# Kernel tuning notes

Measured on AMD Instinct MI355X. Metric: run time of the kernel, lower is better.

Reference implementation:

```python
import jax, jax.numpy as jnp
import numpy as np

B, S, E, H = 2, 2048, 1024, 16
DH = E // H
SCALE = 1.0 / float(np.sqrt(E))  # note: original scales by 1/sqrt(hidden_dim), not head_dim


def _icl_mask(s):
    # triu(diagonal=0) is masked (-inf): only strictly-past positions visible,
    # except (0,0) which is explicitly unmasked so row 0 attends to itself.
    m = jnp.triu(jnp.ones((s, s), dtype=bool), k=0)
    return m.at[0, 0].set(False)


def setup_inputs() -> dict:
    key = jax.random.key(0)
    ks = jax.random.split(key, 7)
    mk = lambda k, shp: jax.random.normal(k, shp, dtype=jnp.float32)
    return {
        "q": mk(ks[0], (B, S, E)),
        "k": mk(ks[1], (B, S, E)),
        "v": mk(ks[2], (B, S, E)),
        "Wq": mk(ks[3], (E, E)) * 0.02,
        "Wk": mk(ks[4], (E, E)) * 0.02,
        "Wv": mk(ks[5], (E, E)) * 0.02,
        "Wo": mk(ks[6], (E, E)) * 0.02,
    }


def reference(q, k, v, Wq, Wk, Wv, Wo):
    b, s, e = q.shape
    h, dh = H, e // H
    # projections (nn.Linear: x @ W.T), split heads -> [b, h, s, dh]
    qh = (q @ Wq.T).reshape(b, s, h, dh).transpose(0, 2, 1, 3)
    kh = (k @ Wk.T).reshape(b, s, h, dh).transpose(0, 2, 1, 3)
    vh = (v @ Wv.T).reshape(b, s, h, dh).transpose(0, 2, 1, 3)
    scores = jnp.einsum("bhsd,bhtd->bhst", qh, kh) * SCALE  # [b,h,s,s]
    scores = jnp.where(_icl_mask(s), -jnp.inf, scores)
    probs = jax.nn.softmax(scores, axis=-1)
    out = jnp.einsum("bhst,bhtd->bhsd", probs, vh)
    out = out.transpose(0, 2, 1, 3).reshape(b, s, e)
    return out @ Wo.T
```

## Files before the change

### kernel.cpp

```cpp
#include <hip/hip_runtime.h>
#include <hip/hip_bf16.h>

typedef unsigned short u16;
typedef unsigned int u32;
typedef __bf16 bf16x8 __attribute__((ext_vector_type(8)));
typedef float float4_ __attribute__((ext_vector_type(4)));

#define B_ 2
#define S_ 2048
#define E_ 1024
#define H_ 16
#define DH_ 64
#define M_ (B_*S_)
#define E2_ (E_*E_)
#define SCALE_ 0.03125f
#define LOG2E_ 1.4426950408889634f

__device__ __forceinline__ u16 f2bf(float f) {
    unsigned int x = __float_as_uint(f);
    x += 0x7fffu + ((x >> 16) & 1u);
    return (u16)(x >> 16);
}

template <typename T> struct raw8;
template <> struct raw8<float> { float4_ lo, hi; };
template <> struct raw8<u16>   { bf16x8 v; };

__device__ __forceinline__ raw8<float> ldr8(const float* p) {
    raw8<float> r; const float4_* q = (const float4_*)p; r.lo = q[0]; r.hi = q[1]; return r;
}
__device__ __forceinline__ raw8<u16> ldr8(const u16* p) {
    raw8<u16> r; r.v = *(const bf16x8*)p; return r;
}
__device__ __forceinline__ bf16x8 cvt8(const raw8<u16>& r) { return r.v; }
__device__ __forceinline__ bf16x8 cvt8(const raw8<float>& r) {
    union { bf16x8 v; __hip_bfloat162 h[4]; } u;
    u.h[0] = __float22bfloat162_rn(float2{r.lo[0], r.lo[1]});
    u.h[1] = __float22bfloat162_rn(float2{r.lo[2], r.lo[3]});
    u.h[2] = __float22bfloat162_rn(float2{r.hi[0], r.hi[1]});
    u.h[3] = __float22bfloat162_rn(float2{r.hi[2], r.hi[3]});
    return u.v;
}
__device__ __forceinline__ bf16x8 ld8(const u16* p) { return *(const bf16x8*)p; }

__device__ __forceinline__ void async16(u16* lds, const u16* g) {
    __builtin_amdgcn_global_load_lds(
        (const __attribute__((address_space(1))) u32*)g,
        (__attribute__((address_space(3))) u32*)lds, 16, 0, 0);
}

__device__ __forceinline__ int swz32(int row, int col) {
    return row * 32 + ((((col >> 3) ^ (row & 3)) << 3) | (col & 7));
}

__global__ __launch_bounds__(256)
void conv_all_kernel(const float* __restrict__ q, const float* __restrict__ k,
                     const float* __restrict__ v,
                     const float* __restrict__ Wq, const float* __restrict__ Wk,
                     const float* __restrict__ Wv, const float* __restrict__ Wo,
                     u16* __restrict__ Xq, u16* __restrict__ Xk, u16* __restrict__ Xv,
                     u16* __restrict__ Wqb, u16* __restrict__ Wkb,
                     u16* __restrict__ Wvb, u16* __restrict__ Wob) {
    const int bid = blockIdx.x;
    const float* src;
    u16* dst;
    size_t base;
    if (bid < 6144) {
        const int which = bid >> 11, off = bid & 2047;
        src = which == 0 ? q : which == 1 ? k : v;
        dst = which == 0 ? Xq : which == 1 ? Xk : Xv;
        base = (size_t)off * 2048;
    } else {
        const int wb = bid - 6144;
        const int which = wb >> 9, off = wb & 511;
        src = which == 0 ? Wq : which == 1 ? Wk : which == 2 ? Wv : Wo;
        dst = which == 0 ? Wqb : which == 1 ? Wkb : which == 2 ? Wvb : Wob;
        base = (size_t)off * 2048;
    }
    const size_t i = base + (size_t)threadIdx.x * 8;
    *(bf16x8*)&dst[i] = cvt8(ldr8(&src[i]));
}

__global__ __launch_bounds__(256)
void proj_kernel(const u16* __restrict__ Xq, const u16* __restrict__ Xk, const u16* __restrict__ Xv,
                 const u16* __restrict__ Wqb, const u16* __restrict__ Wkb, const u16* __restrict__ Wvb,
                 u16* __restrict__ Qh, u16* __restrict__ Kh, u16* __restrict__ Vt) {
    const int z = blockIdx.z;
    const u16* A   = (z == 0) ? Xq : (z == 1) ? Xk : Xv;
    const u16* Wb  = (z == 0) ? Wqb : (z == 1) ? Wkb : Wvb;
    u16* C         = (z == 0) ? Qh : (z == 1) ? Kh : Vt;
    const float cscale = (z == 0) ? SCALE_ : 1.0f;
    const int transV = (z == 2);
    const int bm = blockIdx.x * 128, bn = blockIdx.y * 128;

    __shared__ u16 As[2][128 * 32];
    __shared__ u16 Bs[2][128 * 32];

    const int tid  = threadIdx.x;
    const int lane = tid & 63;
    const int w    = tid >> 6;
    const int wr   = (w >> 1) * 64, wc = (w & 1) * 64;
    const int m16  = lane & 15, quad = lane >> 4, q4 = quad * 4;

    const int row0 = tid >> 2, ch = tid & 3, row1 = row0 + 64;
    const int csw  = ((ch ^ (row0 & 3)) * 8);
    const u16* ag0 = &A[(size_t)(bm + row0) * 1024 + csw];
    const u16* ag1 = &A[(size_t)(bm + row1) * 1024 + csw];
    const u16* wg0 = &Wb[(size_t)(bn + row0) * 1024 + csw];
    const u16* wg1 = &Wb[(size_t)(bn + row1) * 1024 + csw];

    float4_ acc[4][4];
#pragma unroll
    for (int i = 0; i < 4; i++)
#pragma unroll
        for (int j = 0; j < 4; j++) acc[i][j] = (float4_){0.f, 0.f, 0.f, 0.f};

    async16((u16*)((char*)As[0] + (size_t)tid * 16), ag0);
    async16((u16*)((char*)As[0] + (size_t)tid * 16 + 4096), ag1);
    async16((u16*)((char*)Bs[0] + (size_t)tid * 16), wg0);
    async16((u16*)((char*)Bs[0] + (size_t)tid * 16 + 4096), wg1);
    __syncthreads();

    auto step = [&](int t, const u16* Asc, const u16* Bsc, u16* Asn, u16* Bsn) {
        if (t < 31) {
            const size_t ko = (size_t)(t + 1) * 32;
            async16((u16*)((char*)Asn + (size_t)tid * 16), ag0 + ko);
            async16((u16*)((char*)Asn + (size_t)tid * 16 + 4096), ag1 + ko);
            async16((u16*)((char*)Bsn + (size_t)tid * 16), wg0 + ko);
            async16((u16*)((char*)Bsn + (size_t)tid * 16 + 4096), wg1 + ko);
        }
        __builtin_amdgcn_sched_barrier(0);
        bf16x8 af[4], bfr[4];
#pragma unroll
        for (int rt = 0; rt < 4; rt++)
            af[rt] = *(const bf16x8*)&Asc[swz32(wr + rt * 16 + m16, quad * 8)];
#pragma unroll
        for (int ct = 0; ct < 4; ct++)
            bfr[ct] = *(const bf16x8*)&Bsc[swz32(wc + ct * 16 + m16, quad * 8)];
#pragma unroll
        for (int rt = 0; rt < 4; rt++)
#pragma unroll
            for (int ct = 0; ct < 4; ct++)
                acc[rt][ct] = __builtin_amdgcn_mfma_f32_16x16x32_bf16(af[rt], bfr[ct], acc[rt][ct], 0, 0, 0);
        if (t < 31) __syncthreads();
    };

    for (int t = 0; t < 32; t += 2) {
        step(t,     As[0], Bs[0], As[1], Bs[1]);
        step(t + 1, As[1], Bs[1], As[0], Bs[0]);
    }

#pragma unroll
    for (int rt = 0; rt < 4; rt++)
#pragma unroll
        for (int ct = 0; ct < 4; ct++)
#pragma unroll
            for (int r = 0; r < 4; r++) {
                int row = bm + wr + rt * 16 + q4 + r;
                int col = bn + wc + ct * 16 + m16;
                u16 val = f2bf(acc[rt][ct][r] * cscale);
                if (!transV) {
                    C[(size_t)row * 1024 + col] = val;
                } else {
                    int bb = row >> 11, s = row & 2047;
                    C[((size_t)(bb * 1024 + col)) * 2048 + s] = val;
                }
            }
}

__global__ __launch_bounds__(256)
void out_kernel(const u16* __restrict__ AO, const u16* __restrict__ Wob, float* __restrict__ C) {
    const int bm = blockIdx.x * 128, bn = blockIdx.y * 64;

    __shared__ u16 As[2][128 * 32];
    __shared__ u16 Bs[2][64 * 32];

    const int tid  = threadIdx.x;
    const int lane = tid & 63;
    const int w    = tid >> 6;
    const int m16  = lane & 15, quad = lane >> 4, q4 = quad * 4;
    const int c1   = tid + 256;

    const int swc = (((tid & 3) ^ ((tid >> 2) & 3)) * 8);
    const u16* ag0 = &AO[(size_t)(bm + (tid >> 2)) * 1024 + swc];
    const u16* ag1 = &AO[(size_t)(bm + (c1 >> 2)) * 1024 + swc];
    const u16* bg  = &Wob[(size_t)(bn + (tid >> 2)) * 1024 + swc];

    float4_ acc[2][4];
#pragma unroll
    for (int i = 0; i < 2; i++)
#pragma unroll
        for (int j = 0; j < 4; j++) acc[i][j] = (float4_){0.f, 0.f, 0.f, 0.f};

    async16((u16*)((char*)As[0] + (size_t)tid * 16), ag0);
    async16((u16*)((char*)As[0] + (size_t)c1 * 16), ag1);
    async16((u16*)((char*)Bs[0] + (size_t)tid * 16), bg);
    __syncthreads();

    auto step = [&](int t, const u16* Asc, const u16* Bsc, u16* Asn, u16* Bsn) {
        if (t < 31) {
            async16((u16*)((char*)Asn + (size_t)tid * 16), ag0 + (t + 1) * 32);
            async16((u16*)((char*)Asn + (size_t)c1 * 16), ag1 + (t + 1) * 32);
            async16((u16*)((char*)Bsn + (size_t)tid * 16), bg + (t + 1) * 32);
        }
        __builtin_amdgcn_sched_barrier(0);
        bf16x8 af[2], bfr[4];
#pragma unroll
        for (int rt = 0; rt < 2; rt++)
            af[rt] = *(const bf16x8*)&Asc[swz32(w * 32 + rt * 16 + m16, quad * 8)];
#pragma unroll
        for (int ct = 0; ct < 4; ct++)
            bfr[ct] = *(const bf16x8*)&Bsc[swz32(ct * 16 + m16, quad * 8)];
#pragma unroll
        for (int rt = 0; rt < 2; rt++)
#pragma unroll
            for (int ct = 0; ct < 4; ct++)
                acc[rt][ct] = __builtin_amdgcn_mfma_f32_16x16x32_bf16(af[rt], bfr[ct], acc[rt][ct], 0, 0, 0);
        if (t < 31) __syncthreads();
    };

    for (int t = 0; t < 32; t += 2) {
        step(t,     As[0], Bs[0], As[1], Bs[1]);
        step(t + 1, As[1], Bs[1], As[0], Bs[0]);
    }

#pragma unroll
    for (int rt = 0; rt < 2; rt++)
#pragma unroll
        for (int ct = 0; ct < 4; ct++)
#pragma unroll
            for (int r = 0; r < 4; r++) {
                int row = bm + w * 32 + rt * 16 + q4 + r;
                int col = bn + ct * 16 + m16;
                C[(size_t)row * 1024 + col] = acc[rt][ct][r];
            }
}

__device__ __forceinline__ int sw64(int row, int col) {
    return row * 64 + ((((col >> 3) ^ (row & 7)) << 3) | (col & 7));
}

__global__ __launch_bounds__(256, 2)
void attn_kernel(const u16* __restrict__ Qh, const u16* __restrict__ Kh,
                 const u16* __restrict__ Vt, u16* __restrict__ O) {
    const int h    = blockIdx.x;
    const int tq   = 31 - blockIdx.y;
    const int b    = blockIdx.z;
    const int tid  = threadIdx.x;
    const int lane = tid & 63;
    const int w    = tid >> 6;
    const int m16  = lane & 15;
    const int quad = lane >> 4;
    const int q4   = quad * 4;

    __shared__ u16 Ks[3][64 * 64];
    __shared__ u16 Vs[3][64 * 64];
    __shared__ u16 Ps[64 * 64];

    const int srow0 = tid >> 3;
    const int ssw   = (((tid & 7) ^ (srow0 & 7)) * 8);

    const size_t kbase = ((size_t)(b * S_)) * E_ + h * DH_;
    const size_t vbase = ((size_t)(b * 1024 + h * DH_)) * 2048;
    const u16* kg0 = &Kh[kbase + (size_t)srow0 * E_ + ssw];
    const u16* kg1 = kg0 + (size_t)32 * E_;
    const u16* vg0 = &Vt[vbase + (size_t)srow0 * 2048 + ssw];
    const u16* vg1 = vg0 + (size_t)32 * 2048;

    bf16x8 qf[2];
    {
        const u16* qa = Qh + ((size_t)(b * S_ + tq * 64 + w * 16 + m16)) * E_ + h * DH_;
        qf[0] = ld8(qa + quad * 8);
        qf[1] = ld8(qa + 32 + quad * 8);
    }

    float l_part[4] = {0.f, 0.f, 0.f, 0.f};
    float4_ o_acc[4];
#pragma unroll
    for (int dt = 0; dt < 4; dt++) o_acc[dt] = (float4_){0.f, 0.f, 0.f, 0.f};

    u16* k0 = &Ks[0][0]; u16* k1 = &Ks[1][0]; u16* k2 = &Ks[2][0];
    u16* v0 = &Vs[0][0]; u16* v1 = &Vs[1][0]; u16* v2 = &Vs[2][0];

    auto stage_to = [&](u16* kb, u16* vb, int tile) {
        const size_t ko = (size_t)tile * 64 * E_;
        const int    vo = tile * 64;
        async16(kb + tid * 8, kg0 + ko);
        async16(kb + (tid + 256) * 8, kg1 + ko);
        async16(vb + tid * 8, vg0 + vo);
        async16(vb + (tid + 256) * 8, vg1 + vo);
    };

    stage_to(k0, v0, 0);
    stage_to(k1, v1, tq > 0 ? 1 : 0);
    asm volatile("s_waitcnt vmcnt(4)" ::: "memory");
    __builtin_amdgcn_s_barrier();
    __builtin_amdgcn_sched_barrier(0);

    for (int t = 0; t <= tq; t++) {
        stage_to(k2, v2, (t + 2 <= tq) ? (t + 2) : tq);
        __builtin_amdgcn_sched_barrier(0);

        float4_ sc[4];
#pragma unroll
        for (int ct = 0; ct < 4; ct++) sc[ct] = (float4_){0.f, 0.f, 0.f, 0.f};
#pragma unroll
        for (int ks = 0; ks < 2; ks++)
#pragma unroll
            for (int ct = 0; ct < 4; ct++) {
                bf16x8 kf = *(const bf16x8*)&k0[sw64(ct * 16 + m16, ks * 32 + quad * 8)];
                sc[ct] = __builtin_amdgcn_mfma_f32_16x16x32_bf16(qf[ks], kf, sc[ct], 0, 0, 0);
            }

#pragma unroll
        for (int ct = 0; ct < 4; ct++) {
            float pp[4];
            if (t != tq) {
#pragma unroll
                for (int r = 0; r < 4; r++) {
                    pp[r] = exp2f(sc[ct][r] * LOG2E_);
                    l_part[r] += pp[r];
                }
            } else {
#pragma unroll
                for (int r = 0; r < 4; r++) {
                    int i_loc = w * 16 + q4 + r;
                    int j_loc = ct * 16 + m16;
                    bool allow = (j_loc < i_loc) || (tq == 0 && i_loc == 0 && j_loc == 0);
                    pp[r] = allow ? exp2f(sc[ct][r] * LOG2E_) : 0.f;
                    l_part[r] += pp[r];
                }
            }
            union { __hip_bfloat162 h2; u16 s[2]; } u01, u23;
            u01.h2 = __float22bfloat162_rn(float2{pp[0], pp[1]});
            u23.h2 = __float22bfloat162_rn(float2{pp[2], pp[3]});
            Ps[sw64(w * 16 + q4 + 0, ct * 16 + m16)] = u01.s[0];
            Ps[sw64(w * 16 + q4 + 1, ct * 16 + m16)] = u01.s[1];
            Ps[sw64(w * 16 + q4 + 2, ct * 16 + m16)] = u23.s[0];
            Ps[sw64(w * 16 + q4 + 3, ct * 16 + m16)] = u23.s[1];
        }

#pragma unroll
        for (int ks = 0; ks < 2; ks++) {
            bf16x8 pf = *(const bf16x8*)&Ps[sw64(w * 16 + m16, ks * 32 + quad * 8)];
#pragma unroll
            for (int dt = 0; dt < 4; dt++) {
                bf16x8 vf = *(const bf16x8*)&v0[sw64(dt * 16 + m16, ks * 32 + quad * 8)];
                o_acc[dt] = __builtin_amdgcn_mfma_f32_16x16x32_bf16(pf, vf, o_acc[dt], 0, 0, 0);
            }
        }

        asm volatile("s_waitcnt vmcnt(4)" ::: "memory");
        __builtin_amdgcn_s_barrier();
        __builtin_amdgcn_sched_barrier(0);

        u16* tk = k0; k0 = k1; k1 = k2; k2 = tk;
        u16* tv = v0; v0 = v1; v1 = v2; v2 = tv;
    }
    asm volatile("s_waitcnt vmcnt(0)" ::: "memory");

    const size_t obase = ((size_t)(b * S_ + tq * 64)) * E_ + h * DH_;
#pragma unroll
    for (int r = 0; r < 4; r++) {
        float l = l_part[r];
#pragma unroll
        for (int msk = 1; msk <= 8; msk <<= 1) l += __shfl_xor(l, msk);
        float inv_l = 1.0f / l;
        int row = w * 16 + q4 + r;
#pragma unroll
        for (int dt = 0; dt < 4; dt++) {
            int col = dt * 16 + m16;
            O[obase + (size_t)row * E_ + col] = f2bf(o_acc[dt][r] * inv_l);
        }
    }
}

extern "C" void kernel_launch(void* const* d_in, const int* in_sizes, int n_in,
                              void* d_out, int out_size, void* d_ws, size_t ws_size,
                              hipStream_t stream) {
    const float* q  = (const float*)d_in[0];
    const float* k  = (const float*)d_in[1];
    const float* v  = (const float*)d_in[2];
    const float* Wq = (const float*)d_in[3];
    const float* Wk = (const float*)d_in[4];
    const float* Wv = (const float*)d_in[5];
    const float* Wo = (const float*)d_in[6];

    const size_t ME = (size_t)M_ * E_;
    u16* ws  = (u16*)d_ws;
    u16* Qh  = ws;
    u16* Kh  = ws + ME;
    u16* Vt  = ws + 2 * ME;
    u16* AO  = ws + 3 * ME;
    u16* Wqb = AO;
    u16* Wkb = AO + E2_;
    u16* Wvb = AO + 2 * (size_t)E2_;
    u16* Wob = ws + 4 * ME;
    u16* Xv  = ws + 4 * ME + E2_;
    u16* Xq  = (u16*)d_out;
    u16* Xk  = Xq + ME;

    dim3 blk(256);
    conv_all_kernel<<<dim3(8192), blk, 0, stream>>>(q, k, v, Wq, Wk, Wv, Wo,
                                                    Xq, Xk, Xv, Wqb, Wkb, Wvb, Wob);
    proj_kernel<<<dim3(32, 8, 3), blk, 0, stream>>>(Xq, Xk, Xv, Wqb, Wkb, Wvb, Qh, Kh, Vt);
    attn_kernel<<<dim3(16, 32, 2), blk, 0, stream>>>(Qh, Kh, Vt, AO);
    out_kernel<<<dim3(32, 16), blk, 0, stream>>>(AO, Wob, (float*)d_out);
}
```

Baseline: 213.5 us.

## Process KV tiles in pairs with double-buffered pair staging in attention

The attention loop now handles two 64-wide KV tiles per iteration. K and V are staged as double-buffered pairs, and each tile gets its own P buffer, so there is one vmcnt wait and one barrier per pair instead of one per tile. The next pair's loads are issued at the start of each iteration and overlap with two tiles of QK/softmax/PV work. LDS use grows from about 56KB to 80KB per block, which could limit occupancy, and the wait is now a full vmcnt(0) rather than a partial one.

```diff
diff --git a/kernel.cpp b/kernel.cpp
--- a/kernel.cpp
+++ b/kernel.cpp
@@ -253,9 +253,9 @@
     const int quad = lane >> 4;
     const int q4   = quad * 4;
 
-    __shared__ u16 Ks[3][64 * 64];
-    __shared__ u16 Vs[3][64 * 64];
-    __shared__ u16 Ps[64 * 64];
+    __shared__ u16 Ks[2][2][64 * 64];
+    __shared__ u16 Vs[2][2][64 * 64];
+    __shared__ u16 Ps[2][64 * 64];
 
     const int srow0 = tid >> 3;
     const int ssw   = (((tid & 7) ^ (srow0 & 7)) * 8);
@@ -278,9 +278,6 @@
     float4_ o_acc[4];
 #pragma unroll
     for (int dt = 0; dt < 4; dt++) o_acc[dt] = (float4_){0.f, 0.f, 0.f, 0.f};
-
-    u16* k0 = &Ks[0][0]; u16* k1 = &Ks[1][0]; u16* k2 = &Ks[2][0];
-    u16* v0 = &Vs[0][0]; u16* v1 = &Vs[1][0]; u16* v2 = &Vs[2][0];
 
     auto stage_to = [&](u16* kb, u16* vb, int tile) {
         const size_t ko = (size_t)tile * 64 * E_;
@@ -290,28 +287,25 @@
         async16(vb + tid * 8, vg0 + vo);
         async16(vb + (tid + 256) * 8, vg1 + vo);
     };
-
-    stage_to(k0, v0, 0);
-    stage_to(k1, v1, tq > 0 ? 1 : 0);
-    asm volatile("s_waitcnt vmcnt(4)" ::: "memory");
-    __builtin_amdgcn_s_barrier();
-    __builtin_amdgcn_sched_barrier(0);
-
-    for (int t = 0; t <= tq; t++) {
-        stage_to(k2, v2, (t + 2 <= tq) ? (t + 2) : tq);
-        __builtin_amdgcn_sched_barrier(0);
-
-        float4_ sc[4];
+    auto stage_pair = [&](int pp, int t0) {
+        const int ta = (t0     < tq) ? t0     : tq;
+        const int tb = (t0 + 1 < tq) ? t0 + 1 : tq;
+        stage_to(&Ks[pp][0][0], &Vs[pp][0][0], ta);
+        stage_to(&Ks[pp][1][0], &Vs[pp][1][0], tb);
+    };
+
+    auto qk = [&](const u16* Kc, float4_* sc) {
 #pragma unroll
         for (int ct = 0; ct < 4; ct++) sc[ct] = (float4_){0.f, 0.f, 0.f, 0.f};
 #pragma unroll
         for (int ks = 0; ks < 2; ks++)
 #pragma unroll
             for (int ct = 0; ct < 4; ct++) {
-                bf16x8 kf = *(const bf16x8*)&k0[sw64(ct * 16 + m16, ks * 32 + quad * 8)];
+                bf16x8 kf = *(const bf16x8*)&Kc[sw64(ct * 16 + m16, ks * 32 + quad * 8)];
                 sc[ct] = __builtin_amdgcn_mfma_f32_16x16x32_bf16(qf[ks], kf, sc[ct], 0, 0, 0);
             }
-
+    };
+    auto sm = [&](const float4_* sc, u16* Pm, int t) {
 #pragma unroll
         for (int ct = 0; ct < 4; ct++) {
             float pp[4];
@@ -334,30 +328,53 @@
             union { __hip_bfloat162 h2; u16 s[2]; } u01, u23;
             u01.h2 = __float22bfloat162_rn(float2{pp[0], pp[1]});
             u23.h2 = __float22bfloat162_rn(float2{pp[2], pp[3]});
-            Ps[sw64(w * 16 + q4 + 0, ct * 16 + m16)] = u01.s[0];
-            Ps[sw64(w * 16 + q4 + 1, ct * 16 + m16)] = u01.s[1];
-            Ps[sw64(w * 16 + q4 + 2, ct * 16 + m16)] = u23.s[0];
-            Ps[sw64(w * 16 + q4 + 3, ct * 16 + m16)] = u23.s[1];
-        }
-
+            Pm[sw64(w * 16 + q4 + 0, ct * 16 + m16)] = u01.s[0];
+            Pm[sw64(w * 16 + q4 + 1, ct * 16 + m16)] = u01.s[1];
+            Pm[sw64(w * 16 + q4 + 2, ct * 16 + m16)] = u23.s[0];
+            Pm[sw64(w * 16 + q4 + 3, ct * 16 + m16)] = u23.s[1];
+        }
+    };
+    auto pv = [&](const u16* Pm, const u16* Vc) {
 #pragma unroll
         for (int ks = 0; ks < 2; ks++) {
-            bf16x8 pf = *(const bf16x8*)&Ps[sw64(w * 16 + m16, ks * 32 + quad * 8)];
+            bf16x8 pf = *(const bf16x8*)&Pm[sw64(w * 16 + m16, ks * 32 + quad * 8)];
 #pragma unroll
             for (int dt = 0; dt < 4; dt++) {
-                bf16x8 vf = *(const bf16x8*)&v0[sw64(dt * 16 + m16, ks * 32 + quad * 8)];
+                bf16x8 vf = *(const bf16x8*)&Vc[sw64(dt * 16 + m16, ks * 32 + quad * 8)];
                 o_acc[dt] = __builtin_amdgcn_mfma_f32_16x16x32_bf16(pf, vf, o_acc[dt], 0, 0, 0);
             }
         }
-
-        asm volatile("s_waitcnt vmcnt(4)" ::: "memory");
+    };
+
+    stage_pair(0, 0);
+    asm volatile("s_waitcnt vmcnt(0)" ::: "memory");
+    __builtin_amdgcn_s_barrier();
+    __builtin_amdgcn_sched_barrier(0);
+
+    const int npairs = (tq + 2) >> 1;
+    for (int p = 0; p < npairs; p++) {
+        const int cur = p & 1;
+        const int t0 = 2 * p, t1 = 2 * p + 1;
+        const bool have1 = (t1 <= tq);
+
+        stage_pair(cur ^ 1, 2 * p + 2);
+        __builtin_amdgcn_sched_barrier(0);
+
+        float4_ sc0[4], sc1[4];
+        qk(&Ks[cur][0][0], sc0);
+        if (have1) qk(&Ks[cur][1][0], sc1);
+
+        sm(sc0, &Ps[0][0], t0);
+        pv(&Ps[0][0], &Vs[cur][0][0]);
+        if (have1) {
+            sm(sc1, &Ps[1][0], t1);
+            pv(&Ps[1][0], &Vs[cur][1][0]);
+        }
+
+        asm volatile("s_waitcnt vmcnt(0)" ::: "memory");
         __builtin_amdgcn_s_barrier();
         __builtin_amdgcn_sched_barrier(0);
-
-        u16* tk = k0; k0 = k1; k1 = k2; k2 = tk;
-        u16* tv = v0; v0 = v1; v1 = v2; v2 = tv;
-    }
-    asm volatile("s_waitcnt vmcnt(0)" ::: "memory");
+    }
 
     const size_t obase = ((size_t)(b * S_ + tq * 64)) * E_ + h * DH_;
 #pragma unroll
```

Result: no change. 212.5 us (-0.5%).

## Widen attention query tile to 128 rows, two row tiles per wave

Applied to the files above, without the earlier changes.

Each attention block now handles 128 query rows instead of 64, with each wave owning two 16-row tiles, so every staged K/V tile feeds twice as many queries and global K/V traffic per query is halved. The first 64-row half of the block skips the final key tile it does not need. Block order is reversed for one batch and not the other, to pair heavy and light causal blocks. The cost is twice the accumulator registers per wave, a larger P buffer in shared memory, and half as many blocks, which may leave compute units underused or unevenly loaded.

```diff
diff --git a/kernel.cpp b/kernel.cpp
--- a/kernel.cpp
+++ b/kernel.cpp
@@ -244,18 +244,21 @@
 void attn_kernel(const u16* __restrict__ Qh, const u16* __restrict__ Kh,
                  const u16* __restrict__ Vt, u16* __restrict__ O) {
     const int h    = blockIdx.x;
-    const int tq   = 31 - blockIdx.y;
+    const int yy   = blockIdx.y;
     const int b    = blockIdx.z;
+    const int tq2  = b ? yy : 15 - yy;
     const int tid  = threadIdx.x;
     const int lane = tid & 63;
     const int w    = tid >> 6;
+    const int half = w >> 1;
+    const int wq   = w & 1;
     const int m16  = lane & 15;
     const int quad = lane >> 4;
     const int q4   = quad * 4;
 
     __shared__ u16 Ks[3][64 * 64];
     __shared__ u16 Vs[3][64 * 64];
-    __shared__ u16 Ps[64 * 64];
+    __shared__ u16 Ps[2][64 * 64];
 
     const int srow0 = tid >> 3;
     const int ssw   = (((tid & 7) ^ (srow0 & 7)) * 8);
@@ -267,17 +270,23 @@
     const u16* vg0 = &Vt[vbase + (size_t)srow0 * 2048 + ssw];
     const u16* vg1 = vg0 + (size_t)32 * 2048;
 
-    bf16x8 qf[2];
-    {
-        const u16* qa = Qh + ((size_t)(b * S_ + tq * 64 + w * 16 + m16)) * E_ + h * DH_;
-        qf[0] = ld8(qa + quad * 8);
-        qf[1] = ld8(qa + 32 + quad * 8);
-    }
-
-    float l_part[4] = {0.f, 0.f, 0.f, 0.f};
-    float4_ o_acc[4];
-#pragma unroll
-    for (int dt = 0; dt < 4; dt++) o_acc[dt] = (float4_){0.f, 0.f, 0.f, 0.f};
+    bf16x8 qf[2][2];
+#pragma unroll
+    for (int rt = 0; rt < 2; rt++) {
+        const u16* qa = Qh + ((size_t)(b * S_ + tq2 * 128 + half * 64 + wq * 32 + rt * 16 + m16)) * E_ + h * DH_;
+        qf[rt][0] = ld8(qa + quad * 8);
+        qf[rt][1] = ld8(qa + 32 + quad * 8);
+    }
+
+    float l_part[2][4];
+    float4_ o_acc[2][4];
+#pragma unroll
+    for (int rt = 0; rt < 2; rt++)
+#pragma unroll
+        for (int dt = 0; dt < 4; dt++) {
+            o_acc[rt][dt] = (float4_){0.f, 0.f, 0.f, 0.f};
+            l_part[rt][dt] = 0.f;
+        }
 
     u16* k0 = &Ks[0][0]; u16* k1 = &Ks[1][0]; u16* k2 = &Ks[2][0];
     u16* v0 = &Vs[0][0]; u16* v1 = &Vs[1][0]; u16* v2 = &Vs[2][0];
@@ -291,62 +300,73 @@
         async16(vb + (tid + 256) * 8, vg1 + vo);
     };
 
+    const int ktmax  = 2 * tq2 + 1;
+    const int diagkt = 2 * tq2 + half;
+
     stage_to(k0, v0, 0);
-    stage_to(k1, v1, tq > 0 ? 1 : 0);
+    stage_to(k1, v1, 1);
     asm volatile("s_waitcnt vmcnt(4)" ::: "memory");
     __builtin_amdgcn_s_barrier();
     __builtin_amdgcn_sched_barrier(0);
 
-    for (int t = 0; t <= tq; t++) {
-        stage_to(k2, v2, (t + 2 <= tq) ? (t + 2) : tq);
+    for (int kt = 0; kt <= ktmax; kt++) {
+        stage_to(k2, v2, (kt + 2 <= ktmax) ? (kt + 2) : ktmax);
         __builtin_amdgcn_sched_barrier(0);
 
-        float4_ sc[4];
-#pragma unroll
-        for (int ct = 0; ct < 4; ct++) sc[ct] = (float4_){0.f, 0.f, 0.f, 0.f};
-#pragma unroll
-        for (int ks = 0; ks < 2; ks++)
-#pragma unroll
-            for (int ct = 0; ct < 4; ct++) {
-                bf16x8 kf = *(const bf16x8*)&k0[sw64(ct * 16 + m16, ks * 32 + quad * 8)];
-                sc[ct] = __builtin_amdgcn_mfma_f32_16x16x32_bf16(qf[ks], kf, sc[ct], 0, 0, 0);
-            }
-
-#pragma unroll
-        for (int ct = 0; ct < 4; ct++) {
-            float pp[4];
-            if (t != tq) {
-#pragma unroll
-                for (int r = 0; r < 4; r++) {
-                    pp[r] = exp2f(sc[ct][r] * LOG2E_);
-                    l_part[r] += pp[r];
+        if (kt <= diagkt) {
+#pragma unroll
+            for (int rt = 0; rt < 2; rt++) {
+                float4_ sc[4];
+#pragma unroll
+                for (int ct = 0; ct < 4; ct++) sc[ct] = (float4_){0.f, 0.f, 0.f, 0.f};
+#pragma unroll
+                for (int ks = 0; ks < 2; ks++)
+#pragma unroll
+                    for (int ct = 0; ct < 4; ct++) {
+                        bf16x8 kf = *(const bf16x8*)&k0[sw64(ct * 16 + m16, ks * 32 + quad * 8)];
+                        sc[ct] = __builtin_amdgcn_mfma_f32_16x16x32_bf16(qf[rt][ks], kf, sc[ct], 0, 0, 0);
+                    }
+
+                u16* Pm = &Ps[rt][0];
+                const int ihb = wq * 32 + rt * 16 + q4;
+#pragma unroll
+                for (int ct = 0; ct < 4; ct++) {
+                    float pp[4];
+                    if (kt != diagkt) {
+#pragma unroll
+                        for (int r = 0; r < 4; r++) {
+                            pp[r] = exp2f(sc[ct][r] * LOG2E_);
+                            l_part[rt][r] += pp[r];
+                        }
+                    } else {
+#pragma unroll
+                        for (int r = 0; r < 4; r++) {
+                            int i_half = ihb + r;
+                            int j_loc  = ct * 16 + m16;
+                            bool allow = (j_loc < i_half) ||
+                                         (tq2 == 0 && kt == 0 && i_half == 0 && j_loc == 0);
+                            pp[r] = allow ? exp2f(sc[ct][r] * LOG2E_) : 0.f;
+                            l_part[rt][r] += pp[r];
+                        }
+                    }
+                    union { __hip_bfloat162 h2; u16 s[2]; } u01, u23;
+                    u01.h2 = __float22bfloat162_rn(float2{pp[0], pp[1]});
+                    u23.h2 = __float22bfloat162_rn(float2{pp[2], pp[3]});
+                    Pm[sw64(w * 16 + q4 + 0, ct * 16 + m16)] = u01.s[0];
+                    Pm[sw64(w * 16 + q4 + 1, ct * 16 + m16)] = u01.s[1];
+                    Pm[sw64(w * 16 + q4 + 2, ct * 16 + m16)] = u23.s[0];
+                    Pm[sw64(w * 16 + q4 + 3, ct * 16 + m16)] = u23.s[1];
                 }
-            } else {
-#pragma unroll
-                for (int r = 0; r < 4; r++) {
-                    int i_loc = w * 16 + q4 + r;
-                    int j_loc = ct * 16 + m16;
-                    bool allow = (j_loc < i_loc) || (tq == 0 && i_loc == 0 && j_loc == 0);
-                    pp[r] = allow ? exp2f(sc[ct][r] * LOG2E_) : 0.f;
-                    l_part[r] += pp[r];
+
+#pragma unroll
+                for (int ks = 0; ks < 2; ks++) {
+                    bf16x8 pf = *(const bf16x8*)&Pm[sw64(w * 16 + m16, ks * 32 + quad * 8)];
+#pragma unroll
+                    for (int dt = 0; dt < 4; dt++) {
+                        bf16x8 vf = *(const bf16x8*)&v0[sw64(dt * 16 + m16, ks * 32 + quad * 8)];
+                        o_acc[rt][dt] = __builtin_amdgcn_mfma_f32_16x16x32_bf16(pf, vf, o_acc[rt][dt], 0, 0, 0);
+                    }
                 }
-            }
-            union { __hip_bfloat162 h2; u16 s[2]; } u01, u23;
-            u01.h2 = __float22bfloat162_rn(float2{pp[0], pp[1]});
-            u23.h2 = __float22bfloat162_rn(float2{pp[2], pp[3]});
-            Ps[sw64(w * 16 + q4 + 0, ct * 16 + m16)] = u01.s[0];
-            Ps[sw64(w * 16 + q4 + 1, ct * 16 + m16)] = u01.s[1];
-            Ps[sw64(w * 16 + q4 + 2, ct * 16 + m16)] = u23.s[0];
-            Ps[sw64(w * 16 + q4 + 3, ct * 16 + m16)] = u23.s[1];
-        }
-
-#pragma unroll
-        for (int ks = 0; ks < 2; ks++) {
-            bf16x8 pf = *(const bf16x8*)&Ps[sw64(w * 16 + m16, ks * 32 + quad * 8)];
-#pragma unroll
-            for (int dt = 0; dt < 4; dt++) {
-                bf16x8 vf = *(const bf16x8*)&v0[sw64(dt * 16 + m16, ks * 32 + quad * 8)];
-                o_acc[dt] = __builtin_amdgcn_mfma_f32_16x16x32_bf16(pf, vf, o_acc[dt], 0, 0, 0);
             }
         }
 
@@ -359,18 +379,21 @@
     }
     asm volatile("s_waitcnt vmcnt(0)" ::: "memory");
 
-    const size_t obase = ((size_t)(b * S_ + tq * 64)) * E_ + h * DH_;
-#pragma unroll
-    for (int r = 0; r < 4; r++) {
-        float l = l_part[r];
-#pragma unroll
-        for (int msk = 1; msk <= 8; msk <<= 1) l += __shfl_xor(l, msk);
-        float inv_l = 1.0f / l;
-        int row = w * 16 + q4 + r;
-#pragma unroll
-        for (int dt = 0; dt < 4; dt++) {
-            int col = dt * 16 + m16;
-            O[obase + (size_t)row * E_ + col] = f2bf(o_acc[dt][r] * inv_l);
+#pragma unroll
+    for (int rt = 0; rt < 2; rt++) {
+        const size_t obase = ((size_t)(b * S_ + tq2 * 128 + half * 64 + wq * 32 + rt * 16)) * E_ + h * DH_;
+#pragma unroll
+        for (int r = 0; r < 4; r++) {
+            float l = l_part[rt][r];
+#pragma unroll
+            for (int msk = 1; msk <= 8; msk <<= 1) l += __shfl_xor(l, msk);
+            float inv_l = 1.0f / l;
+            int row = q4 + r;
+#pragma unroll
+            for (int dt = 0; dt < 4; dt++) {
+                int col = dt * 16 + m16;
+                O[obase + (size_t)row * E_ + col] = f2bf(o_acc[rt][dt][r] * inv_l);
+            }
         }
     }
 }
@@ -404,6 +427,6 @@
     conv_all_kernel<<<dim3(8192), blk, 0, stream>>>(q, k, v, Wq, Wk, Wv, Wo,
                                                     Xq, Xk, Xv, Wqb, Wkb, Wvb, Wob);
     proj_kernel<<<dim3(32, 8, 3), blk, 0, stream>>>(Xq, Xk, Xv, Wqb, Wkb, Wvb, Qh, Kh, Vt);
-    attn_kernel<<<dim3(16, 32, 2), blk, 0, stream>>>(Qh, Kh, Vt, AO);
+    attn_kernel<<<dim3(16, 16, 2), blk, 0, stream>>>(Qh, Kh, Vt, AO);
     out_kernel<<<dim3(32, 16), blk, 0, stream>>>(AO, Wob, (float*)d_out);
 }
```

After: 224.0 us. 1.05x slower.

## Triple-buffer GEMM shared-memory tiles with partial vmcnt waits in projection kernels

Applied to the files above, without the earlier changes.

Changes the projection and output GEMM kernels from double to triple buffering of the LDS K-tiles. Each iteration issues the load two steps ahead and waits only until the next tile has landed (partial vmcnt), not for all outstanding loads. This is meant to hide global-to-LDS latency better than a full __syncthreads per step. It costs 50% more shared memory per block, which may reduce occupancy, and adds redundant loads of tile 31 at the tail.

```diff
diff --git a/kernel.cpp b/kernel.cpp
--- a/kernel.cpp
+++ b/kernel.cpp
@@ -93,8 +93,8 @@
     const int transV = (z == 2);
     const int bm = blockIdx.x * 128, bn = blockIdx.y * 128;
 
-    __shared__ u16 As[2][128 * 32];
-    __shared__ u16 Bs[2][128 * 32];
+    __shared__ u16 As[3][128 * 32];
+    __shared__ u16 Bs[3][128 * 32];
 
     const int tid  = threadIdx.x;
     const int lane = tid & 63;
@@ -102,12 +102,12 @@
     const int wr   = (w >> 1) * 64, wc = (w & 1) * 64;
     const int m16  = lane & 15, quad = lane >> 4, q4 = quad * 4;
 
-    const int row0 = tid >> 2, ch = tid & 3, row1 = row0 + 64;
+    const int row0 = tid >> 2, ch = tid & 3;
     const int csw  = ((ch ^ (row0 & 3)) * 8);
     const u16* ag0 = &A[(size_t)(bm + row0) * 1024 + csw];
-    const u16* ag1 = &A[(size_t)(bm + row1) * 1024 + csw];
+    const u16* ag1 = &A[(size_t)(bm + row0 + 64) * 1024 + csw];
     const u16* wg0 = &Wb[(size_t)(bn + row0) * 1024 + csw];
-    const u16* wg1 = &Wb[(size_t)(bn + row1) * 1024 + csw];
+    const u16* wg1 = &Wb[(size_t)(bn + row0 + 64) * 1024 + csw];
 
     float4_ acc[4][4];
 #pragma unroll
@@ -115,40 +115,48 @@
 #pragma unroll
         for (int j = 0; j < 4; j++) acc[i][j] = (float4_){0.f, 0.f, 0.f, 0.f};
 
-    async16((u16*)((char*)As[0] + (size_t)tid * 16), ag0);
-    async16((u16*)((char*)As[0] + (size_t)tid * 16 + 4096), ag1);
-    async16((u16*)((char*)Bs[0] + (size_t)tid * 16), wg0);
-    async16((u16*)((char*)Bs[0] + (size_t)tid * 16 + 4096), wg1);
-    __syncthreads();
-
-    auto step = [&](int t, const u16* Asc, const u16* Bsc, u16* Asn, u16* Bsn) {
-        if (t < 31) {
-            const size_t ko = (size_t)(t + 1) * 32;
-            async16((u16*)((char*)Asn + (size_t)tid * 16), ag0 + ko);
-            async16((u16*)((char*)Asn + (size_t)tid * 16 + 4096), ag1 + ko);
-            async16((u16*)((char*)Bsn + (size_t)tid * 16), wg0 + ko);
-            async16((u16*)((char*)Bsn + (size_t)tid * 16 + 4096), wg1 + ko);
-        }
-        __builtin_amdgcn_sched_barrier(0);
+    u16* A0 = &As[0][0]; u16* A1 = &As[1][0]; u16* A2 = &As[2][0];
+    u16* B0 = &Bs[0][0]; u16* B1 = &Bs[1][0]; u16* B2 = &Bs[2][0];
+
+    auto stage = [&](u16* Ab, u16* Bb, int t) {
+        const size_t ko = (size_t)t * 32;
+        async16((u16*)((char*)Ab + (size_t)tid * 16), ag0 + ko);
+        async16((u16*)((char*)Ab + (size_t)tid * 16 + 4096), ag1 + ko);
+        async16((u16*)((char*)Bb + (size_t)tid * 16), wg0 + ko);
+        async16((u16*)((char*)Bb + (size_t)tid * 16 + 4096), wg1 + ko);
+    };
+
+    stage(A0, B0, 0);
+    stage(A1, B1, 1);
+    asm volatile("s_waitcnt vmcnt(4)" ::: "memory");
+    __builtin_amdgcn_s_barrier();
+    __builtin_amdgcn_sched_barrier(0);
+
+    for (int t = 0; t < 32; t++) {
+        stage(A2, B2, (t + 2 < 32) ? (t + 2) : 31);
+        __builtin_amdgcn_sched_barrier(0);
+
         bf16x8 af[4], bfr[4];
 #pragma unroll
         for (int rt = 0; rt < 4; rt++)
-            af[rt] = *(const bf16x8*)&Asc[swz32(wr + rt * 16 + m16, quad * 8)];
+            af[rt] = *(const bf16x8*)&A0[swz32(wr + rt * 16 + m16, quad * 8)];
 #pragma unroll
         for (int ct = 0; ct < 4; ct++)
-            bfr[ct] = *(const bf16x8*)&Bsc[swz32(wc + ct * 16 + m16, quad * 8)];
+            bfr[ct] = *(const bf16x8*)&B0[swz32(wc + ct * 16 + m16, quad * 8)];
 #pragma unroll
         for (int rt = 0; rt < 4; rt++)
 #pragma unroll
             for (int ct = 0; ct < 4; ct++)
                 acc[rt][ct] = __builtin_amdgcn_mfma_f32_16x16x32_bf16(af[rt], bfr[ct], acc[rt][ct], 0, 0, 0);
-        if (t < 31) __syncthreads();
-    };
-
-    for (int t = 0; t < 32; t += 2) {
-        step(t,     As[0], Bs[0], As[1], Bs[1]);
-        step(t + 1, As[1], Bs[1], As[0], Bs[0]);
-    }
+
+        asm volatile("s_waitcnt vmcnt(4)" ::: "memory");
+        __builtin_amdgcn_s_barrier();
+        __builtin_amdgcn_sched_barrier(0);
+
+        u16* ta = A0; A0 = A1; A1 = A2; A2 = ta;
+        u16* tb = B0; B0 = B1; B1 = B2; B2 = tb;
+    }
+    asm volatile("s_waitcnt vmcnt(0)" ::: "memory");
 
 #pragma unroll
     for (int rt = 0; rt < 4; rt++)
@@ -172,8 +180,8 @@
 void out_kernel(const u16* __restrict__ AO, const u16* __restrict__ Wob, float* __restrict__ C) {
     const int bm = blockIdx.x * 128, bn = blockIdx.y * 64;
 
-    __shared__ u16 As[2][128 * 32];
-    __shared__ u16 Bs[2][64 * 32];
+    __shared__ u16 As[3][128 * 32];
+    __shared__ u16 Bs[3][64 * 32];
 
     const int tid  = threadIdx.x;
     const int lane = tid & 63;
@@ -192,37 +200,47 @@
 #pragma unroll
         for (int j = 0; j < 4; j++) acc[i][j] = (float4_){0.f, 0.f, 0.f, 0.f};
 
-    async16((u16*)((char*)As[0] + (size_t)tid * 16), ag0);
-    async16((u16*)((char*)As[0] + (size_t)c1 * 16), ag1);
-    async16((u16*)((char*)Bs[0] + (size_t)tid * 16), bg);
-    __syncthreads();
-
-    auto step = [&](int t, const u16* Asc, const u16* Bsc, u16* Asn, u16* Bsn) {
-        if (t < 31) {
-            async16((u16*)((char*)Asn + (size_t)tid * 16), ag0 + (t + 1) * 32);
-            async16((u16*)((char*)Asn + (size_t)c1 * 16), ag1 + (t + 1) * 32);
-            async16((u16*)((char*)Bsn + (size_t)tid * 16), bg + (t + 1) * 32);
-        }
-        __builtin_amdgcn_sched_barrier(0);
+    u16* A0 = &As[0][0]; u16* A1 = &As[1][0]; u16* A2 = &As[2][0];
+    u16* B0 = &Bs[0][0]; u16* B1 = &Bs[1][0]; u16* B2 = &Bs[2][0];
+
+    auto stage = [&](u16* Ab, u16* Bb, int t) {
+        const size_t ko = (size_t)t * 32;
+        async16((u16*)((char*)Ab + (size_t)tid * 16), ag0 + ko);
+        async16((u16*)((char*)Ab + (size_t)c1 * 16), ag1 + ko);
+        async16((u16*)((char*)Bb + (size_t)tid * 16), bg + ko);
+    };
+
+    stage(A0, B0, 0);
+    stage(A1, B1, 1);
+    asm volatile("s_waitcnt vmcnt(3)" ::: "memory");
+    __builtin_amdgcn_s_barrier();
+    __builtin_amdgcn_sched_barrier(0);
+
+    for (int t = 0; t < 32; t++) {
+        stage(A2, B2, (t + 2 < 32) ? (t + 2) : 31);
+        __builtin_amdgcn_sched_barrier(0);
+
         bf16x8 af[2], bfr[4];
 #pragma unroll
         for (int rt = 0; rt < 2; rt++)
-            af[rt] = *(const bf16x8*)&Asc[swz32(w * 32 + rt * 16 + m16, quad * 8)];
+            af[rt] = *(const bf16x8*)&A0[swz32(w * 32 + rt * 16 + m16, quad * 8)];
 #pragma unroll
         for (int ct = 0; ct < 4; ct++)
-            bfr[ct] = *(const bf16x8*)&Bsc[swz32(ct * 16 + m16, quad * 8)];
+            bfr[ct] = *(const bf16x8*)&B0[swz32(ct * 16 + m16, quad * 8)];
 #pragma unroll
         for (int rt = 0; rt < 2; rt++)
 #pragma unroll
             for (int ct = 0; ct < 4; ct++)
                 acc[rt][ct] = __builtin_amdgcn_mfma_f32_16x16x32_bf16(af[rt], bfr[ct], acc[rt][ct], 0, 0, 0);
-        if (t < 31) __syncthreads();
-    };
-
-    for (int t = 0; t < 32; t += 2) {
-        step(t,     As[0], Bs[0], As[1], Bs[1]);
-        step(t + 1, As[1], Bs[1], As[0], Bs[0]);
-    }
+
+        asm volatile("s_waitcnt vmcnt(3)" ::: "memory");
+        __builtin_amdgcn_s_barrier();
+        __builtin_amdgcn_sched_barrier(0);
+
+        u16* ta = A0; A0 = A1; A1 = A2; A2 = ta;
+        u16* tb = B0; B0 = B1; B1 = B2; B2 = tb;
+    }
+    asm volatile("s_waitcnt vmcnt(0)" ::: "memory");
 
 #pragma unroll
     for (int rt = 0; rt < 2; rt++)
```

After: 213.4 us. About the same (-0.1%).
